# Optimization experiments

Measured on AMD Instinct MI355X. Metric: run time of the kernel, lower is better.

## Reference

```python
import jax, jax.numpy as jnp
import numpy as np

UNITS = 1024
IN_DIM = 1024
BATCH = 64
SEQ = 512


def setup_inputs() -> dict:
    key = jax.random.key(0)
    k_x, k_wf, k_wb = jax.random.split(key, 3)
    x = jax.random.normal(k_x, (BATCH, SEQ, IN_DIM), dtype=jnp.float32)
    # keras 'random_normal' initializer -> stddev 0.05
    W_fwd = jax.random.normal(k_wf, (IN_DIM + UNITS, 4 * UNITS), dtype=jnp.float32) * 0.05
    b_fwd = jnp.zeros((4 * UNITS,), dtype=jnp.float32)
    W_bwd = jax.random.normal(k_wb, (IN_DIM + UNITS, 4 * UNITS), dtype=jnp.float32) * 0.05
    b_bwd = jnp.zeros((4 * UNITS,), dtype=jnp.float32)
    return {"x": x, "W_fwd": W_fwd, "b_fwd": b_fwd, "W_bwd": W_bwd, "b_bwd": b_bwd}


def _lstm_scan(x_tbd, W, b, units, reverse):
    # x_tbd: [T, B, D] time-major
    B = x_tbd.shape[1]
    h0 = jnp.zeros((B, units), dtype=x_tbd.dtype)
    c0 = jnp.zeros((B, units), dtype=x_tbd.dtype)

    def step(carry, x_t):
        h, c = carry
        z = jnp.concatenate([x_t, h], axis=-1) @ W + b  # [B, 4U]
        zi, zf, zo, zg = jnp.split(z, 4, axis=-1)
        c_new = jax.nn.sigmoid(zf) * c + jax.nn.sigmoid(zi) * jnp.tanh(zg)
        h_new = jax.nn.sigmoid(zo) * jnp.tanh(c_new)
        return (h_new, c_new), h_new

    _, hs = jax.lax.scan(step, (h0, c0), x_tbd, reverse=reverse)
    return hs  # [T, B, U], aligned with input time order


def reference(x, W_fwd, b_fwd, W_bwd, b_bwd):
    x_tbd = jnp.transpose(x, (1, 0, 2))  # [T, B, D]
    h_fwd = _lstm_scan(x_tbd, W_fwd, b_fwd, UNITS, reverse=False)
    h_bwd = _lstm_scan(x_tbd, W_bwd, b_bwd, UNITS, reverse=True)
    h = jnp.concatenate([h_fwd, h_bwd], axis=-1)  # [T, B, 2U]
    return jnp.transpose(h, (1, 0, 2))  # [B, T, 2U]
```

## Files before the change

### kernel.cpp

```cpp
#include <hip/hip_runtime.h>
#include <stdint.h>

#define B_ 64
#define T_ 512
#define D_ 1024
#define U_ 1024
#define G4_ 4096
#define M_ (B_ * T_)

typedef unsigned short u16;
typedef float f32x4 __attribute__((ext_vector_type(4)));
typedef _Float16 f16x8 __attribute__((ext_vector_type(8)));
typedef unsigned short u16x4 __attribute__((ext_vector_type(4)));

__device__ __forceinline__ u16 f2h(float f) {
  union { _Float16 h; u16 u; } v; v.h = (_Float16)f; return v.u;
}
__device__ __forceinline__ float h2f(u16 u) {
  union { _Float16 h; u16 u; } v; v.u = u; return (float)v.h;
}
__device__ __forceinline__ float sigm(float x) { return 1.f / (1.f + __expf(-x)); }
__device__ __forceinline__ float tanhf_(float x) {
  x = fminf(12.f, fmaxf(-12.f, x));
  float e = __expf(2.f * x);
  return (e - 1.f) / (e + 1.f);
}

__device__ __forceinline__ void glds16(const void* g, void* l) {
  __builtin_amdgcn_global_load_lds(
      (const __attribute__((address_space(1))) uint32_t*)g,
      (__attribute__((address_space(3))) uint32_t*)l, 16, 0, 0);
}

template <int R>
__device__ __forceinline__ void stage_tile(const char* gbase, long gs, char* lds, int tid) {
  const int lane = tid & 63, wid = tid >> 6;
#pragma unroll
  for (int j = wid; j < R / 8; j += 4) {
    const int row = j * 8 + (lane >> 3);
    const int lg = ((lane & 7) * 16) ^ ((row & 7) << 4);
    glds16(gbase + (long)row * gs + lg, lds + j * 1024);
  }
}

__device__ __forceinline__ f16x8 read_frag(const char* lds, int row, int kbyte) {
  const int ph = row * 128 + (kbyte ^ ((row & 7) << 4));
  return *(const f16x8*)(lds + ph);
}

#define MFMA_(a, b, c) __builtin_amdgcn_mfma_f32_16x16x32_f16(a, b, c, 0, 0, 0)


__global__ __launch_bounds__(256) void cast_x_kernel(const float* __restrict__ x,
                                                     u16* __restrict__ xb) {
  const long n = (long)M_ * D_ / 4;
  for (long i = (long)blockIdx.x * blockDim.x + threadIdx.x; i < n;
       i += (long)gridDim.x * blockDim.x) {
    f32x4 v = ((const f32x4*)x)[i];
    u16x4 r;
#pragma unroll
    for (int j = 0; j < 4; ++j) r[j] = f2h(v[j]);
    ((u16x4*)xb)[i] = r;
  }
}

__global__ __launch_bounds__(256) void pack_w_kernel(const float* __restrict__ Wf,
                                                     const float* __restrict__ Wb,
                                                     u16* __restrict__ wxT,
                                                     u16* __restrict__ whT) {
  const int idx = blockIdx.x * 256 + threadIdx.x;
  const int p = idx & 4095;
  const int kc = (idx >> 12) & 63;
  const int part = (idx >> 18) & 1;
  const int d = (idx >> 19) & 1;
  const float* W = d ? Wb : Wf;
  const int orig = ((p >> 4) & 3) * 1024 + ((p >> 6) << 4) + (p & 15);
  u16* dst = (part ? whT : wxT) + ((long)d * G4_ + p) * 1024 + kc * 16;
  const float* src = W + ((long)(part * 1024 + kc * 16)) * G4_ + orig;
#pragma unroll
  for (int j = 0; j < 16; ++j) dst[j] = f2h(src[(long)j * G4_]);
}

__global__ __launch_bounds__(256) void gemm_xproj2(const u16* __restrict__ xbf,
                                                   const u16* __restrict__ wT,
                                                   const float* __restrict__ bF,
                                                   const float* __restrict__ bB,
                                                   u16* __restrict__ xp2) {
  __shared__ __align__(16) char smem[64 * 1024];
  const int tid = threadIdx.x, lane = tid & 63, wid = tid >> 6;
  const int wr = wid >> 1, wc = wid & 1;
  const int tm = blockIdx.x * 128, tn = blockIdx.y * 128, d = blockIdx.z;
  const char* Ag = (const char*)xbf + (long)tm * 2048;
  const char* Bg = (const char*)wT + ((long)d * G4_ + tn) * 2048;

  f32x4 acc[4][4];
#pragma unroll
  for (int mi = 0; mi < 4; ++mi)
#pragma unroll
    for (int ni = 0; ni < 4; ++ni)
#pragma unroll
      for (int v = 0; v < 4; ++v) acc[mi][ni][v] = 0.f;

  stage_tile<128>(Ag, 2048, smem, tid);
  stage_tile<128>(Bg, 2048, smem + 32768, tid);
  __syncthreads();
  const int rA = lane & 15, kb = (lane >> 4) * 16;

  for (int cc = 0; cc < 16; ++cc) {
    const int cur = cc & 1;
    char* Ac = smem + cur * 16384;
    char* Bc = smem + 32768 + cur * 16384;
    if (cc + 1 < 16) {
      stage_tile<128>(Ag + (cc + 1) * 128, 2048, smem + (cur ^ 1) * 16384, tid);
      stage_tile<128>(Bg + (cc + 1) * 128, 2048, smem + 32768 + (cur ^ 1) * 16384, tid);
    }
    f16x8 aF[4][2], bFr[4][2];
#pragma unroll
    for (int mi = 0; mi < 4; ++mi)
#pragma unroll
      for (int ks = 0; ks < 2; ++ks)
        aF[mi][ks] = read_frag(Ac, wr * 64 + mi * 16 + rA, kb + ks * 64);
#pragma unroll
    for (int ni = 0; ni < 4; ++ni)
#pragma unroll
      for (int ks = 0; ks < 2; ++ks)
        bFr[ni][ks] = read_frag(Bc, wc * 64 + ni * 16 + rA, kb + ks * 64);
#pragma unroll
    for (int mi = 0; mi < 4; ++mi)
#pragma unroll
      for (int ni = 0; ni < 4; ++ni)
#pragma unroll
        for (int ks = 0; ks < 2; ++ks)
          acc[mi][ni] = MFMA_(aF[mi][ks], bFr[ni][ks], acc[mi][ni]);
    __syncthreads();
  }

  const float* bias = d ? bB : bF;
#pragma unroll
  for (int ni = 0; ni < 4; ++ni) {
    const int p = tn + wc * 64 + ni * 16 + rA;
    const int orig = ((p >> 4) & 3) * 1024 + ((p >> 6) << 4) + (p & 15);
    const float bv = bias[orig];
    const int ub2 = p >> 6, pl = p & 63;
#pragma unroll
    for (int mi = 0; mi < 4; ++mi) {
      const int m0 = tm + wr * 64 + mi * 16 + (lane >> 4) * 4;
#pragma unroll
      for (int v = 0; v < 4; ++v) {
        const int m = m0 + v, b = m >> 9, t = m & 511;
        const int bh = b >> 5, br = b & 31;
        xp2[(((((long)d * T_ + t) * 64 + ub2) * 2 + bh) * 32 + br) * 64 + pl] =
            f2h(acc[mi][ni][v] + bv);
      }
    }
  }
}


__device__ __forceinline__ void stage_hA(const char* g, char* lds, int tid) {
  const int lane = tid & 63, wid = tid >> 6;
#pragma unroll
  for (int q = 0; q < 16; ++q) {
    const int idx = wid + q * 4;
    const int row = idx * 8 + (lane >> 3);
    const int off = ((lane & 7) * 16) ^ (((row >> 4) & 7) << 4);
    glds16(g + (long)row * 128 + off, lds + idx * 1024);
  }
}

__device__ __forceinline__ void stage_Bchunk(const char* wbase, int cc, char* slot, int tid) {
  const int lane = tid & 63, wid = tid >> 6;
#pragma unroll
  for (int q = 0; q < 4; ++q) {
    const int idx = wid + q * 4;
    const int row = idx * 8 + (lane >> 3);
    const int off = ((lane & 7) * 16) ^ (((row >> 1) & 7) << 4);
    glds16(wbase + (long)(row >> 1) * 2048 + cc * 256 + (row & 1) * 128 + off,
           slot + idx * 1024);
  }
}

__device__ __forceinline__ void stage_xpb(const char* g, char* lds, int tid) {
  const int lane = tid & 63, wid = tid >> 6;
  glds16(g + wid * 1024 + lane * 16 - lane * 16 + (long)lane * 16, lds + wid * 1024);
}

template <int CC>
__device__ __forceinline__ void kstep(char* smem, const char* wbase, int tid,
                                      int wr, int wc, int rA, int kq,
                                      f32x4 (&acc)[2]) {
  constexpr int REM = 7 - CC;
  constexpr int N = 4 * (REM < 3 ? REM : 3);
  asm volatile("s_waitcnt vmcnt(%0)" :: "i"(N) : "memory");
  __builtin_amdgcn_s_barrier();
  asm volatile("" ::: "memory");
  const char* A = smem;
  const char* Bslot = smem + 65536 + (CC & 3) * 16384;
  f16x8 aF[4], bF[2][4];
  const int br = wr * 16 + rA;
#pragma unroll
  for (int ks = 0; ks < 4; ++ks) {
    const int kbyte = CC * 256 + ks * 64 + kq * 16;
    aF[ks] = *(const f16x8*)(A + br * 2048 + (kbyte ^ ((br & 7) << 4)));
  }
#pragma unroll
  for (int ni = 0; ni < 2; ++ni) {
    const int pi = wc * 32 + ni * 16 + rA;
#pragma unroll
    for (int ks = 0; ks < 4; ++ks) {
      const int kb2 = ks * 64 + kq * 16;
      bF[ni][ks] = *(const f16x8*)(Bslot + pi * 256 + (kb2 ^ ((pi & 7) << 4)));
    }
  }
#pragma unroll
  for (int ni = 0; ni < 2; ++ni)
#pragma unroll
    for (int ks = 0; ks < 4; ++ks)
      acc[ni] = MFMA_(aF[ks], bF[ni][ks], acc[ni]);
  asm volatile("s_waitcnt lgkmcnt(0)" ::: "memory");
  __builtin_amdgcn_sched_barrier(0);
  __builtin_amdgcn_s_barrier();
  asm volatile("" ::: "memory");
  if (CC + 4 < 8)
    stage_Bchunk(wbase, CC + 4, smem + 65536 + ((CC + 4) & 3) * 16384, tid);
}

__global__ __launch_bounds__(256) void lstm_step2(
    const u16* __restrict__ whT, const u16* __restrict__ xp2,
    const u16* __restrict__ h_read, u16* __restrict__ h_write,
    float* __restrict__ c_state, float* __restrict__ out, int s) {
  __shared__ __align__(16) char smem[143360];
  const int tid = threadIdx.x, lane = tid & 63, wid = tid >> 6;
  const int wr = wid >> 1, wc = wid & 1, rA = lane & 15, kq = lane >> 4;
  const int g = blockIdx.x, ub = g >> 1, d = g & 1, bh = blockIdx.y;
  const int t = d ? (T_ - 1 - s) : s;
  const char* hA = (const char*)h_read + ((long)d * B_ + bh * 32) * 2048;
  const char* wbase = (const char*)whT + ((long)d * G4_ + ub * 64) * 2048;
  const char* xg = (const char*)xp2 + ((((long)d * T_ + t) * 64 + ub) * 2 + bh) * 4096;
  char* xpb = smem + 131072;
  float* zbuf = (float*)(smem + 135168);

  stage_xpb(xg, xpb, tid);
  stage_hA(hA, smem, tid);
#pragma unroll
  for (int c0 = 0; c0 < 4; ++c0)
    stage_Bchunk(wbase, c0, smem + 65536 + c0 * 16384, tid);

  f32x4 acc[2];
#pragma unroll
  for (int ni = 0; ni < 2; ++ni)
#pragma unroll
    for (int v = 0; v < 4; ++v) acc[ni][v] = 0.f;

  kstep<0>(smem, wbase, tid, wr, wc, rA, kq, acc);
  kstep<1>(smem, wbase, tid, wr, wc, rA, kq, acc);
  kstep<2>(smem, wbase, tid, wr, wc, rA, kq, acc);
  kstep<3>(smem, wbase, tid, wr, wc, rA, kq, acc);
  kstep<4>(smem, wbase, tid, wr, wc, rA, kq, acc);
  kstep<5>(smem, wbase, tid, wr, wc, rA, kq, acc);
  kstep<6>(smem, wbase, tid, wr, wc, rA, kq, acc);
  kstep<7>(smem, wbase, tid, wr, wc, rA, kq, acc);

#pragma unroll
  for (int ni = 0; ni < 2; ++ni)
#pragma unroll
    for (int v = 0; v < 4; ++v) {
      const int row = wr * 16 + kq * 4 + v;
      const int col = wc * 32 + ni * 16 + rA;
      zbuf[row * 64 + col] = acc[ni][v];
    }
  __syncthreads();

  const u16* xph = (const u16*)xpb;
#pragma unroll
  for (int j = 0; j < 2; ++j) {
    const int o = tid * 2 + j, bl = o >> 4, ui = o & 15;
    const float zi = zbuf[bl * 64 + ui]      + h2f(xph[bl * 64 + ui]);
    const float zf = zbuf[bl * 64 + 16 + ui] + h2f(xph[bl * 64 + 16 + ui]);
    const float zo = zbuf[bl * 64 + 32 + ui] + h2f(xph[bl * 64 + 32 + ui]);
    const float zg = zbuf[bl * 64 + 48 + ui] + h2f(xph[bl * 64 + 48 + ui]);
    const int bglob = bh * 32 + bl, u = ub * 16 + ui;
    const long ci = ((long)d * B_ + bglob) * 1024 + u;
    const float c = c_state[ci];
    const float i_ = sigm(zi), ff = sigm(zf), o_ = sigm(zo), g_ = tanhf_(zg);
    const float cn = ff * c + i_ * g_;
    const float hn = o_ * tanhf_(cn);
    c_state[ci] = cn;
    h_write[ci] = f2h(hn);
    out[((long)bglob * T_ + t) * 2048 + d * 1024 + u] = hn;
  }
}

__global__ __launch_bounds__(256) void lstm_step_fused(
    const u16* __restrict__ whT, const u16* __restrict__ wxT,
    const u16* __restrict__ xbf,
    const float* __restrict__ bF, const float* __restrict__ bB,
    const u16* __restrict__ h_read, u16* __restrict__ h_write,
    float* __restrict__ c_state, float* __restrict__ out, int s) {
  __shared__ __align__(16) char smem[32 * 1024];
  float* zbuf = (float*)smem;
  const int tid = threadIdx.x, lane = tid & 63, wid = tid >> 6;
  const int wr = wid >> 1, wc = wid & 1;
  const int ub = blockIdx.x, d = blockIdx.y;
  const int t = d ? (T_ - 1 - s) : s;
  const char* hA = (const char*)(h_read + (long)d * B_ * U_);
  const char* Bh = (const char*)(whT + ((long)d * G4_ + ub * 64) * 1024);
  const char* xA = (const char*)xbf + (long)t * (D_ * 2);
  const char* Bx = (const char*)(wxT + ((long)d * G4_ + ub * 64) * 1024);

  auto stage = [&](int cc, int buf) {
    char* Ad = smem + buf * 8192;
    char* Bd = smem + 16384 + buf * 8192;
    if (cc < 16) {
      stage_tile<64>(hA + cc * 128, U_ * 2, Ad, tid);
      stage_tile<64>(Bh + cc * 128, 1024 * 2, Bd, tid);
    } else {
      const int cx = cc - 16;
      stage_tile<64>(xA + cx * 128, (long)T_ * D_ * 2, Ad, tid);
      stage_tile<64>(Bx + cx * 128, 1024 * 2, Bd, tid);
    }
  };

  f32x4 acc[2][2];
#pragma unroll
  for (int mi = 0; mi < 2; ++mi)
#pragma unroll
    for (int ni = 0; ni < 2; ++ni)
#pragma unroll
      for (int v = 0; v < 4; ++v) acc[mi][ni][v] = 0.f;

  stage(0, 0);
  __syncthreads();
  const int rA = lane & 15, kb = (lane >> 4) * 16;

  for (int cc = 0; cc < 32; ++cc) {
    const int cur = cc & 1;
    char* Ac = smem + cur * 8192;
    char* Bc = smem + 16384 + cur * 8192;
    if (cc + 1 < 32) stage(cc + 1, cur ^ 1);
    f16x8 aF[2][2], bFr[2][2];
#pragma unroll
    for (int mi = 0; mi < 2; ++mi)
#pragma unroll
      for (int ks = 0; ks < 2; ++ks)
        aF[mi][ks] = read_frag(Ac, wr * 32 + mi * 16 + rA, kb + ks * 64);
#pragma unroll
    for (int ni = 0; ni < 2; ++ni)
#pragma unroll
      for (int ks = 0; ks < 2; ++ks)
        bFr[ni][ks] = read_frag(Bc, wc * 32 + ni * 16 + rA, kb + ks * 64);
#pragma unroll
    for (int mi = 0; mi < 2; ++mi)
#pragma unroll
      for (int ni = 0; ni < 2; ++ni)
#pragma unroll
        for (int ks = 0; ks < 2; ++ks)
          acc[mi][ni] = MFMA_(aF[mi][ks], bFr[ni][ks], acc[mi][ni]);
    __syncthreads();
  }

#pragma unroll
  for (int mi = 0; mi < 2; ++mi)
#pragma unroll
    for (int ni = 0; ni < 2; ++ni)
#pragma unroll
      for (int v = 0; v < 4; ++v) {
        const int row = wr * 32 + mi * 16 + (lane >> 4) * 4 + v;
        const int col = wc * 32 + ni * 16 + rA;
        zbuf[row * 64 + col] = acc[mi][ni][v];
      }
  __syncthreads();

  const int b = tid >> 2, u0 = (tid & 3) * 4;
  const float* bias = d ? bB : bF;
#pragma unroll
  for (int j = 0; j < 4; ++j) {
    const int ui = u0 + j, u = ub * 16 + ui;
    float zi = zbuf[b * 64 + ui] + bias[u];
    float zf = zbuf[b * 64 + 16 + ui] + bias[1024 + u];
    float zo = zbuf[b * 64 + 32 + ui] + bias[2048 + u];
    float zg = zbuf[b * 64 + 48 + ui] + bias[3072 + u];
    const long ci = (((long)d * B_ + b) << 10) + u;
    const float c = c_state[ci];
    const float i_ = sigm(zi), ff = sigm(zf), o_ = sigm(zo), g_ = tanhf_(zg);
    const float cn = ff * c + i_ * g_;
    const float hn = o_ * tanhf_(cn);
    c_state[ci] = cn;
    h_write[ci] = f2h(hn);
    out[(((long)b * T_ + t) << 11) + ((long)d << 10) + u] = hn;
  }
}


extern "C" void kernel_launch(void* const* d_in, const int* in_sizes, int n_in,
                              void* d_out, int out_size, void* d_ws, size_t ws_size,
                              hipStream_t stream) {
  const float* x = (const float*)d_in[0];
  const float* Wf = (const float*)d_in[1];
  const float* bfp = (const float*)d_in[2];
  const float* Wb = (const float*)d_in[3];
  const float* bbp = (const float*)d_in[4];
  float* out = (float*)d_out;
  char* ws = (char*)d_ws;

  size_t off = 0;
  auto alloc = [&](size_t bytes) {
    char* p = ws + off;
    off = (off + bytes + 255) & ~(size_t)255;
    return p;
  };
  u16* xbf = (u16*)alloc((size_t)M_ * D_ * 2);
  u16* wxT = (u16*)alloc((size_t)2 * G4_ * 1024 * 2);
  u16* whT = (u16*)alloc((size_t)2 * G4_ * 1024 * 2);
  u16* hst = (u16*)alloc((size_t)2 * 2 * B_ * U_ * 2);
  float* cst = (float*)alloc((size_t)2 * B_ * U_ * 4);
  const size_t base_need = off;
  const size_t xproj_bytes = (size_t)2 * B_ * T_ * G4_ * 2;
  const bool fused = (ws_size < base_need + xproj_bytes + 256);
  u16* xproj = fused ? nullptr : (u16*)alloc(xproj_bytes);

  hipMemsetAsync(hst, 0, (size_t)2 * 2 * B_ * U_ * 2, stream);
  hipMemsetAsync(cst, 0, (size_t)2 * B_ * U_ * 4, stream);

  cast_x_kernel<<<2048, 256, 0, stream>>>(x, xbf);
  pack_w_kernel<<<4096, 256, 0, stream>>>(Wf, Wb, wxT, whT);

  if (!fused) {
    dim3 gg(M_ / 128, G4_ / 128, 2);
    gemm_xproj2<<<gg, 256, 0, stream>>>(xbf, wxT, bfp, bbp, xproj);
    for (int s = 0; s < T_; ++s) {
      const u16* hr = hst + (size_t)(s & 1) * 2 * B_ * U_;
      u16* hw = hst + (size_t)((s + 1) & 1) * 2 * B_ * U_;
      lstm_step2<<<dim3(128, 2), 256, 0, stream>>>(whT, xproj, hr, hw, cst, out, s);
    }
  } else {
    for (int s = 0; s < T_; ++s) {
      const u16* hr = hst + (size_t)(s & 1) * 2 * B_ * U_;
      u16* hw = hst + (size_t)((s + 1) & 1) * 2 * B_ * U_;
      lstm_step_fused<<<dim3(64, 2), 256, 0, stream>>>(whT, wxT, xbf, bfp, bbp,
                                                       hr, hw, cst, out, s);
    }
  }
}
```

Before: 4.164 ms.

## Pre-swizzle recurrent weights into fragment layout and load xproj directly to registers

Recurrent weights are packed into a fragment-ordered layout, so each B chunk is one contiguous 16-byte-per-lane copy into LDS and the MFMA fragment reads need no XOR swizzle. The x-projection slice and the cell state are now loaded straight into registers early in the step instead of being staged through LDS, and the epilogue handles two units per thread with vectorized stores. The z buffer is padded to a 65-float row stride to cut LDS bank conflicts. The fused fallback for small workspaces is removed, so the kernel now always needs the full xproj allocation.

Measured after the change: 3.999 ms. 4.0% less time.

```diff
diff --git a/kernel.cpp b/kernel.cpp
--- a/kernel.cpp
+++ b/kernel.cpp
@@ -7,6 +7,7 @@
 #define U_ 1024
 #define G4_ 4096
 #define M_ (B_ * T_)
+#define ZLD 65
 
 typedef unsigned short u16;
 typedef float f32x4 __attribute__((ext_vector_type(4)));
@@ -16,8 +17,8 @@
 __device__ __forceinline__ u16 f2h(float f) {
   union { _Float16 h; u16 u; } v; v.h = (_Float16)f; return v.u;
 }
-__device__ __forceinline__ float h2f(u16 u) {
-  union { _Float16 h; u16 u; } v; v.u = u; return (float)v.h;
+__device__ __forceinline__ float h2f(uint32_t u) {
+  union { _Float16 h; u16 u; } v; v.u = (u16)u; return (float)v.h;
 }
 __device__ __forceinline__ float sigm(float x) { return 1.f / (1.f + __expf(-x)); }
 __device__ __forceinline__ float tanhf_(float x) {
@@ -64,21 +65,38 @@
   }
 }
 
-__global__ __launch_bounds__(256) void pack_w_kernel(const float* __restrict__ Wf,
-                                                     const float* __restrict__ Wb,
-                                                     u16* __restrict__ wxT,
-                                                     u16* __restrict__ whT) {
+__global__ __launch_bounds__(256) void pack_wx_kernel(const float* __restrict__ Wf,
+                                                      const float* __restrict__ Wb,
+                                                      u16* __restrict__ wxT) {
   const int idx = blockIdx.x * 256 + threadIdx.x;
   const int p = idx & 4095;
   const int kc = (idx >> 12) & 63;
-  const int part = (idx >> 18) & 1;
+  const int d = (idx >> 18) & 1;
+  const float* W = d ? Wb : Wf;
+  const int orig = ((p >> 4) & 3) * 1024 + ((p >> 6) << 4) + (p & 15);
+  u16* dst = wxT + ((long)d * G4_ + p) * 1024 + kc * 16;
+  const float* src = W + (long)(kc * 16) * G4_ + orig;
+#pragma unroll
+  for (int j = 0; j < 16; ++j) dst[j] = f2h(src[(long)j * G4_]);
+}
+
+__global__ __launch_bounds__(256) void pack_whfl_kernel(const float* __restrict__ Wf,
+                                                        const float* __restrict__ Wb,
+                                                        u16* __restrict__ whfl) {
+  const int idx = blockIdx.x * 256 + threadIdx.x;
+  const int l = idx & 63;
+  const int f = (idx >> 6) & 15;
+  const int cc = (idx >> 10) & 7;
+  const int ub = (idx >> 13) & 63;
   const int d = (idx >> 19) & 1;
   const float* W = d ? Wb : Wf;
-  const int orig = ((p >> 4) & 3) * 1024 + ((p >> 6) << 4) + (p & 15);
-  u16* dst = (part ? whT : wxT) + ((long)d * G4_ + p) * 1024 + kc * 16;
-  const float* src = W + ((long)(part * 1024 + kc * 16)) * G4_ + orig;
-#pragma unroll
-  for (int j = 0; j < 16; ++j) dst[j] = f2h(src[(long)j * G4_]);
+  const int ni = f >> 2, kkl = f & 3;
+  const int ocol = ni * 1024 + ub * 16 + (l & 15);
+  const int krow = 1024 + cc * 128 + kkl * 32 + (l >> 4) * 8;
+  u16* dst = whfl + ((((long)(d * 64 + ub) * 8 + cc) * 16 + f) << 9) + l * 8;
+  const float* src = W + (long)krow * G4_ + ocol;
+#pragma unroll
+  for (int j = 0; j < 8; ++j) dst[j] = f2h(src[(long)j * G4_]);
 }
 
 __global__ __launch_bounds__(256) void gemm_xproj2(const u16* __restrict__ xbf,
@@ -168,25 +186,17 @@
   }
 }
 
-__device__ __forceinline__ void stage_Bchunk(const char* wbase, int cc, char* slot, int tid) {
+__device__ __forceinline__ void stage_Bc(const char* wfl, int cc, char* slot, int tid) {
   const int lane = tid & 63, wid = tid >> 6;
 #pragma unroll
   for (int q = 0; q < 4; ++q) {
-    const int idx = wid + q * 4;
-    const int row = idx * 8 + (lane >> 3);
-    const int off = ((lane & 7) * 16) ^ (((row >> 1) & 7) << 4);
-    glds16(wbase + (long)(row >> 1) * 2048 + cc * 256 + (row & 1) * 128 + off,
-           slot + idx * 1024);
-  }
-}
-
-__device__ __forceinline__ void stage_xpb(const char* g, char* lds, int tid) {
-  const int lane = tid & 63, wid = tid >> 6;
-  glds16(g + wid * 1024 + lane * 16 - lane * 16 + (long)lane * 16, lds + wid * 1024);
+    const int f = wid * 4 + q;
+    glds16(wfl + (long)cc * 16384 + f * 1024 + lane * 16, slot + f * 1024);
+  }
 }
 
 template <int CC>
-__device__ __forceinline__ void kstep(char* smem, const char* wbase, int tid,
+__device__ __forceinline__ void kstep(char* smem, const char* wfl, int tid,
                                       int wr, int wc, int rA, int kq,
                                       f32x4 (&acc)[2]) {
   constexpr int REM = 7 - CC;
@@ -196,6 +206,7 @@
   asm volatile("" ::: "memory");
   const char* A = smem;
   const char* Bslot = smem + 65536 + (CC & 3) * 16384;
+  const int lane16 = (tid & 63) << 4;
   f16x8 aF[4], bF[2][4];
   const int br = wr * 16 + rA;
 #pragma unroll
@@ -204,14 +215,10 @@
     aF[ks] = *(const f16x8*)(A + br * 2048 + (kbyte ^ ((br & 7) << 4)));
   }
 #pragma unroll
-  for (int ni = 0; ni < 2; ++ni) {
-    const int pi = wc * 32 + ni * 16 + rA;
-#pragma unroll
-    for (int ks = 0; ks < 4; ++ks) {
-      const int kb2 = ks * 64 + kq * 16;
-      bF[ni][ks] = *(const f16x8*)(Bslot + pi * 256 + (kb2 ^ ((pi & 7) << 4)));
-    }
-  }
+  for (int ni = 0; ni < 2; ++ni)
+#pragma unroll
+    for (int ks = 0; ks < 4; ++ks)
+      bF[ni][ks] = *(const f16x8*)(Bslot + ((wc * 2 + ni) * 4 + ks) * 1024 + lane16);
 #pragma unroll
   for (int ni = 0; ni < 2; ++ni)
 #pragma unroll
@@ -222,29 +229,41 @@
   __builtin_amdgcn_s_barrier();
   asm volatile("" ::: "memory");
   if (CC + 4 < 8)
-    stage_Bchunk(wbase, CC + 4, smem + 65536 + ((CC + 4) & 3) * 16384, tid);
-}
-
-__global__ __launch_bounds__(256) void lstm_step2(
-    const u16* __restrict__ whT, const u16* __restrict__ xp2,
+    stage_Bc(wfl, CC + 4, smem + 65536 + ((CC + 4) & 3) * 16384, tid);
+}
+
+__global__ __launch_bounds__(256) void lstm_step8(
+    const u16* __restrict__ whfl, const u16* __restrict__ xp2,
     const u16* __restrict__ h_read, u16* __restrict__ h_write,
-    float* __restrict__ c_state, float* __restrict__ out, int s) {
-  __shared__ __align__(16) char smem[143360];
+    float* __restrict__ cst, float* __restrict__ out, int s) {
+  __shared__ __align__(16) char smem[131072 + ZLD * 32 * 4];
+  float* zbuf = (float*)(smem + 131072);
   const int tid = threadIdx.x, lane = tid & 63, wid = tid >> 6;
-  const int wr = wid >> 1, wc = wid & 1, rA = lane & 15, kq = lane >> 4;
+  const int wr = wid >> 1, wc = wid & 1;
   const int g = blockIdx.x, ub = g >> 1, d = g & 1, bh = blockIdx.y;
   const int t = d ? (T_ - 1 - s) : s;
   const char* hA = (const char*)h_read + ((long)d * B_ + bh * 32) * 2048;
-  const char* wbase = (const char*)whT + ((long)d * G4_ + ub * 64) * 2048;
+  const char* wfl = (const char*)whfl + ((long)(d * 64 + ub) << 17);
   const char* xg = (const char*)xp2 + ((((long)d * T_ + t) * 64 + ub) * 2 + bh) * 4096;
-  char* xpb = smem + 131072;
-  float* zbuf = (float*)(smem + 135168);
-
-  stage_xpb(xg, xpb, tid);
+  const int rA = lane & 15, kq = lane >> 4;
+
+  const int bl_g = tid >> 3, ui_g = (tid & 7) * 2;
+  const int u_g = ub * 16 + ui_g;
+  const int bglob = bh * 32 + bl_g;
+
+  uint32_t xr[4];
+  const char* xt = xg + (bl_g * 64 + ui_g) * 2;
+#define XL(gg)                                                          \
+  asm volatile("global_load_dword %0, %1, off offset:%2"               \
+               : "=v"(xr[gg]) : "v"(xt), "n"(gg * 32) : "memory")
+  XL(0); XL(1); XL(2); XL(3);
+#undef XL
   stage_hA(hA, smem, tid);
 #pragma unroll
   for (int c0 = 0; c0 < 4; ++c0)
-    stage_Bchunk(wbase, c0, smem + 65536 + c0 * 16384, tid);
+    stage_Bc(wfl, c0, smem + 65536 + c0 * 16384, tid);
+
+  const float2 creg = *(const float2*)(cst + ((long)d * B_ + bglob) * 1024 + u_g);
 
   f32x4 acc[2];
 #pragma unroll
@@ -252,142 +271,46 @@
 #pragma unroll
     for (int v = 0; v < 4; ++v) acc[ni][v] = 0.f;
 
-  kstep<0>(smem, wbase, tid, wr, wc, rA, kq, acc);
-  kstep<1>(smem, wbase, tid, wr, wc, rA, kq, acc);
-  kstep<2>(smem, wbase, tid, wr, wc, rA, kq, acc);
-  kstep<3>(smem, wbase, tid, wr, wc, rA, kq, acc);
-  kstep<4>(smem, wbase, tid, wr, wc, rA, kq, acc);
-  kstep<5>(smem, wbase, tid, wr, wc, rA, kq, acc);
-  kstep<6>(smem, wbase, tid, wr, wc, rA, kq, acc);
-  kstep<7>(smem, wbase, tid, wr, wc, rA, kq, acc);
+  kstep<0>(smem, wfl, tid, wr, wc, rA, kq, acc);
+  kstep<1>(smem, wfl, tid, wr, wc, rA, kq, acc);
+  kstep<2>(smem, wfl, tid, wr, wc, rA, kq, acc);
+  kstep<3>(smem, wfl, tid, wr, wc, rA, kq, acc);
+  kstep<4>(smem, wfl, tid, wr, wc, rA, kq, acc);
+  kstep<5>(smem, wfl, tid, wr, wc, rA, kq, acc);
+  kstep<6>(smem, wfl, tid, wr, wc, rA, kq, acc);
+  kstep<7>(smem, wfl, tid, wr, wc, rA, kq, acc);
 
 #pragma unroll
   for (int ni = 0; ni < 2; ++ni)
 #pragma unroll
     for (int v = 0; v < 4; ++v) {
       const int row = wr * 16 + kq * 4 + v;
-      const int col = wc * 32 + ni * 16 + rA;
-      zbuf[row * 64 + col] = acc[ni][v];
+      const int col = (wc * 2 + ni) * 16 + rA;
+      zbuf[row * ZLD + col] = acc[ni][v];
     }
   __syncthreads();
 
-  const u16* xph = (const u16*)xpb;
-#pragma unroll
-  for (int j = 0; j < 2; ++j) {
-    const int o = tid * 2 + j, bl = o >> 4, ui = o & 15;
-    const float zi = zbuf[bl * 64 + ui]      + h2f(xph[bl * 64 + ui]);
-    const float zf = zbuf[bl * 64 + 16 + ui] + h2f(xph[bl * 64 + 16 + ui]);
-    const float zo = zbuf[bl * 64 + 32 + ui] + h2f(xph[bl * 64 + 32 + ui]);
-    const float zg = zbuf[bl * 64 + 48 + ui] + h2f(xph[bl * 64 + 48 + ui]);
-    const int bglob = bh * 32 + bl, u = ub * 16 + ui;
-    const long ci = ((long)d * B_ + bglob) * 1024 + u;
-    const float c = c_state[ci];
-    const float i_ = sigm(zi), ff = sigm(zf), o_ = sigm(zo), g_ = tanhf_(zg);
-    const float cn = ff * c + i_ * g_;
-    const float hn = o_ * tanhf_(cn);
-    c_state[ci] = cn;
-    h_write[ci] = f2h(hn);
-    out[((long)bglob * T_ + t) * 2048 + d * 1024 + u] = hn;
-  }
-}
-
-__global__ __launch_bounds__(256) void lstm_step_fused(
-    const u16* __restrict__ whT, const u16* __restrict__ wxT,
-    const u16* __restrict__ xbf,
-    const float* __restrict__ bF, const float* __restrict__ bB,
-    const u16* __restrict__ h_read, u16* __restrict__ h_write,
-    float* __restrict__ c_state, float* __restrict__ out, int s) {
-  __shared__ __align__(16) char smem[32 * 1024];
-  float* zbuf = (float*)smem;
-  const int tid = threadIdx.x, lane = tid & 63, wid = tid >> 6;
-  const int wr = wid >> 1, wc = wid & 1;
-  const int ub = blockIdx.x, d = blockIdx.y;
-  const int t = d ? (T_ - 1 - s) : s;
-  const char* hA = (const char*)(h_read + (long)d * B_ * U_);
-  const char* Bh = (const char*)(whT + ((long)d * G4_ + ub * 64) * 1024);
-  const char* xA = (const char*)xbf + (long)t * (D_ * 2);
-  const char* Bx = (const char*)(wxT + ((long)d * G4_ + ub * 64) * 1024);
-
-  auto stage = [&](int cc, int buf) {
-    char* Ad = smem + buf * 8192;
-    char* Bd = smem + 16384 + buf * 8192;
-    if (cc < 16) {
-      stage_tile<64>(hA + cc * 128, U_ * 2, Ad, tid);
-      stage_tile<64>(Bh + cc * 128, 1024 * 2, Bd, tid);
-    } else {
-      const int cx = cc - 16;
-      stage_tile<64>(xA + cx * 128, (long)T_ * D_ * 2, Ad, tid);
-      stage_tile<64>(Bx + cx * 128, 1024 * 2, Bd, tid);
-    }
-  };
-
-  f32x4 acc[2][2];
-#pragma unroll
-  for (int mi = 0; mi < 2; ++mi)
-#pragma unroll
-    for (int ni = 0; ni < 2; ++ni)
-#pragma unroll
-      for (int v = 0; v < 4; ++v) acc[mi][ni][v] = 0.f;
-
-  stage(0, 0);
-  __syncthreads();
-  const int rA = lane & 15, kb = (lane >> 4) * 16;
-
-  for (int cc = 0; cc < 32; ++cc) {
-    const int cur = cc & 1;
-    char* Ac = smem + cur * 8192;
-    char* Bc = smem + 16384 + cur * 8192;
-    if (cc + 1 < 32) stage(cc + 1, cur ^ 1);
-    f16x8 aF[2][2], bFr[2][2];
-#pragma unroll
-    for (int mi = 0; mi < 2; ++mi)
-#pragma unroll
-      for (int ks = 0; ks < 2; ++ks)
-        aF[mi][ks] = read_frag(Ac, wr * 32 + mi * 16 + rA, kb + ks * 64);
-#pragma unroll
-    for (int ni = 0; ni < 2; ++ni)
-#pragma unroll
-      for (int ks = 0; ks < 2; ++ks)
-        bFr[ni][ks] = read_frag(Bc, wc * 32 + ni * 16 + rA, kb + ks * 64);
-#pragma unroll
-    for (int mi = 0; mi < 2; ++mi)
-#pragma unroll
-      for (int ni = 0; ni < 2; ++ni)
-#pragma unroll
-        for (int ks = 0; ks < 2; ++ks)
-          acc[mi][ni] = MFMA_(aF[mi][ks], bFr[ni][ks], acc[mi][ni]);
-    __syncthreads();
-  }
-
-#pragma unroll
-  for (int mi = 0; mi < 2; ++mi)
-#pragma unroll
-    for (int ni = 0; ni < 2; ++ni)
-#pragma unroll
-      for (int v = 0; v < 4; ++v) {
-        const int row = wr * 32 + mi * 16 + (lane >> 4) * 4 + v;
-        const int col = wc * 32 + ni * 16 + rA;
-        zbuf[row * 64 + col] = acc[mi][ni][v];
-      }
-  __syncthreads();
-
-  const int b = tid >> 2, u0 = (tid & 3) * 4;
-  const float* bias = d ? bB : bF;
-#pragma unroll
-  for (int j = 0; j < 4; ++j) {
-    const int ui = u0 + j, u = ub * 16 + ui;
-    float zi = zbuf[b * 64 + ui] + bias[u];
-    float zf = zbuf[b * 64 + 16 + ui] + bias[1024 + u];
-    float zo = zbuf[b * 64 + 32 + ui] + bias[2048 + u];
-    float zg = zbuf[b * 64 + 48 + ui] + bias[3072 + u];
-    const long ci = (((long)d * B_ + b) << 10) + u;
-    const float c = c_state[ci];
-    const float i_ = sigm(zi), ff = sigm(zf), o_ = sigm(zo), g_ = tanhf_(zg);
-    const float cn = ff * c + i_ * g_;
-    const float hn = o_ * tanhf_(cn);
-    c_state[ci] = cn;
-    h_write[ci] = f2h(hn);
-    out[(((long)b * T_ + t) << 11) + ((long)d << 10) + u] = hn;
+  {
+    const float* zb = zbuf + bl_g * ZLD + ui_g;
+    const float zi0 = zb[0]  + h2f(xr[0] & 0xffff);
+    const float zi1 = zb[1]  + h2f(xr[0] >> 16);
+    const float zf0 = zb[16] + h2f(xr[1] & 0xffff);
+    const float zf1 = zb[17] + h2f(xr[1] >> 16);
+    const float zo0 = zb[32] + h2f(xr[2] & 0xffff);
+    const float zo1 = zb[33] + h2f(xr[2] >> 16);
+    const float zg0 = zb[48] + h2f(xr[3] & 0xffff);
+    const float zg1 = zb[49] + h2f(xr[3] >> 16);
+    const float cn0 = sigm(zf0) * creg.x + sigm(zi0) * tanhf_(zg0);
+    const float cn1 = sigm(zf1) * creg.y + sigm(zi1) * tanhf_(zg1);
+    const float hn0 = sigm(zo0) * tanhf_(cn0);
+    const float hn1 = sigm(zo1) * tanhf_(cn1);
+
+    float2 cw; cw.x = cn0; cw.y = cn1;
+    *(float2*)(cst + ((long)d * B_ + bglob) * 1024 + u_g) = cw;
+    const uint32_t hv = (uint32_t)f2h(hn0) | ((uint32_t)f2h(hn1) << 16);
+    *(uint32_t*)(h_write + ((long)d * B_ + bglob) * 1024 + u_g) = hv;
+    float2 o2; o2.x = hn0; o2.y = hn1;
+    *(float2*)(out + ((long)bglob * T_ + t) * 2048 + d * 1024 + u_g) = o2;
   }
 }
 
@@ -411,34 +334,24 @@
   };
   u16* xbf = (u16*)alloc((size_t)M_ * D_ * 2);
   u16* wxT = (u16*)alloc((size_t)2 * G4_ * 1024 * 2);
-  u16* whT = (u16*)alloc((size_t)2 * G4_ * 1024 * 2);
+  u16* whfl = (u16*)alloc((size_t)2 * 64 * 128 * 1024);
   u16* hst = (u16*)alloc((size_t)2 * 2 * B_ * U_ * 2);
   float* cst = (float*)alloc((size_t)2 * B_ * U_ * 4);
-  const size_t base_need = off;
-  const size_t xproj_bytes = (size_t)2 * B_ * T_ * G4_ * 2;
-  const bool fused = (ws_size < base_need + xproj_bytes + 256);
-  u16* xproj = fused ? nullptr : (u16*)alloc(xproj_bytes);
+  u16* xproj = (u16*)alloc((size_t)2 * B_ * T_ * G4_ * 2);
 
   hipMemsetAsync(hst, 0, (size_t)2 * 2 * B_ * U_ * 2, stream);
   hipMemsetAsync(cst, 0, (size_t)2 * B_ * U_ * 4, stream);
 
   cast_x_kernel<<<2048, 256, 0, stream>>>(x, xbf);
-  pack_w_kernel<<<4096, 256, 0, stream>>>(Wf, Wb, wxT, whT);
-
-  if (!fused) {
-    dim3 gg(M_ / 128, G4_ / 128, 2);
-    gemm_xproj2<<<gg, 256, 0, stream>>>(xbf, wxT, bfp, bbp, xproj);
-    for (int s = 0; s < T_; ++s) {
-      const u16* hr = hst + (size_t)(s & 1) * 2 * B_ * U_;
-      u16* hw = hst + (size_t)((s + 1) & 1) * 2 * B_ * U_;
-      lstm_step2<<<dim3(128, 2), 256, 0, stream>>>(whT, xproj, hr, hw, cst, out, s);
-    }
-  } else {
-    for (int s = 0; s < T_; ++s) {
-      const u16* hr = hst + (size_t)(s & 1) * 2 * B_ * U_;
-      u16* hw = hst + (size_t)((s + 1) & 1) * 2 * B_ * U_;
-      lstm_step_fused<<<dim3(64, 2), 256, 0, stream>>>(whT, wxT, xbf, bfp, bbp,
-                                                       hr, hw, cst, out, s);
-    }
-  }
-}
+  pack_wx_kernel<<<2048, 256, 0, stream>>>(Wf, Wb, wxT);
+  pack_whfl_kernel<<<4096, 256, 0, stream>>>(Wf, Wb, whfl);
+
+  dim3 gg(M_ / 128, G4_ / 128, 2);
+  gemm_xproj2<<<gg, 256, 0, stream>>>(xbf, wxT, bfp, bbp, xproj);
+
+  for (int s = 0; s < T_; ++s) {
+    const u16* hr = hst + (size_t)(s & 1) * 2 * B_ * U_;
+    u16* hw = hst + (size_t)((s + 1) & 1) * 2 * B_ * U_;
+    lstm_step8<<<dim3(128, 2), 256, 0, stream>>>(whfl, xproj, hr, hw, cst, out, s);
+  }
+}
```
